# Kernel optimization log

Hardware: AMD Instinct MI355X
Metric: run time of the kernel (lower is better)

Reference implementation:

```python
import jax, jax.numpy as jnp
import numpy as np

KAPPA = 8
TEMP = 200.0
EPS = 1e-15
N, E, D, T = 8192, 131072, 128, 8
P0, P1 = 512, 128
ZI = D - KAPPA  # non-kappa feature dims


def expmap0(u):
    # Poincare ball exp map at origin, c=1
    n = jnp.clip(jnp.linalg.norm(u, axis=-1, keepdims=True), EPS)
    return jnp.tanh(n) * u / n


def logmap0(y):
    # Poincare ball log map at origin, c=1 (clipped for numerical safety)
    n = jnp.clip(jnp.linalg.norm(y, axis=-1, keepdims=True), EPS)
    t = jnp.clip(n, EPS, 1.0 - 1e-5)
    return jnp.arctanh(t) * y / n


def setup_inputs() -> dict:
    key = jax.random.key(0)
    ks = jax.random.split(key, 8)
    g = lambda k, shp: jax.random.normal(k, shp, jnp.float32) / np.float32(np.sqrt(shp[0]))
    return {
        "x": 0.1 * jax.random.normal(ks[0], (N, D), jnp.float32),
        "y": jax.random.normal(ks[1], (T, N), jnp.float32),
        "We0": g(ks[2], (ZI, ZI)), "be0": jnp.zeros((ZI,), jnp.float32),
        "Ws0": g(ks[3], (D, P0)), "bs0": jnp.zeros((P0,), jnp.float32),
        "We1": g(ks[4], (ZI, ZI)), "be1": jnp.zeros((ZI,), jnp.float32),
        "Ws1": g(ks[5], (D, P1)), "bs1": jnp.zeros((P1,), jnp.float32),
        "adj": jax.random.randint(ks[6], (2, E), 0, N),
    }


def _embed_pool(z, agg, We, be, Ws, bs):
    # embed_pool: keep z0, message-pass zi; compute cluster scores s (hyperbolic head)
    z0, zi = z[:, :KAPPA], z[:, KAPPA:]
    zi = agg(zi @ We + be)
    s = expmap0(agg(z @ Ws + bs))
    z = jnp.concatenate([z0, zi], axis=-1)
    S = jax.nn.softmax(logmap0(s) * TEMP, axis=0)  # soft assignment over nodes
    return z, S


def reference(x, y, We0, be0, Ws0, bs0, We1, be1, Ws1, bs1, adj):
    n = x.shape[0]
    # dense adjacency at level 0 (as in the original renorm)
    A0 = jnp.zeros((n, n), x.dtype).at[adj[0], adj[1]].set(1.0)
    # sparse aggregation equivalent to A0 @ h
    agg0 = lambda h: jax.ops.segment_sum(h[adj[1]], adj[0], num_segments=n)

    # ---- level 0 ----
    z, S0 = _embed_pool(x, agg0, We0, be0, Ws0, bs0)
    x1 = jnp.einsum('ij,ik->jk', S0, z)        # [P0, D] pooled features
    y1 = jnp.einsum('ij,ki->kj', S0, y)        # [T, P0] pooled targets
    A1 = jnp.einsum('ji,jk,kl->il', S0, A0, S0)  # [P0, P0] coarsened adjacency
    loss_ent = jax.scipy.special.entr(S0).sum()

    # ---- level 1 (dense weighted adjacency, i.e. dense_to_coo(A1) round trip) ----
    agg1 = lambda h: A1 @ h
    z1, S1 = _embed_pool(x1, agg1, We1, be1, Ws1, bs1)
    x2 = jnp.einsum('ij,ik->jk', S1, z1)       # [P1, D]
    y2 = jnp.einsum('ij,ki->kj', S1, y1)       # [T, P1]
    loss_ent = loss_ent + jax.scipy.special.entr(S1).sum()

    z_r = jnp.concatenate([x, x1, x2], axis=0)   # [N+P0+P1, D]
    y_r = jnp.concatenate([y, y1, y2], axis=-1)  # [T, N+P0+P1]
    return z_r, y_r, loss_ent
```

## Files before the change

### kernel.cpp

```cpp
#include <hip/hip_runtime.h>
#include <hip/hip_bf16.h>

#define NC   8192
#define EC   131072
#define DC   128
#define TC   8
#define P0C  512
#define P1C  128
#define ZIC  120
#define NCAT 248
#define TEMPC 200.0f
#define ATANH_MAX 6.1053405f

typedef short short8 __attribute__((ext_vector_type(8)));
typedef float f32x4 __attribute__((ext_vector_type(4)));

__device__ inline unsigned short f2b(float f) {
  union { float f; unsigned u; } x; x.f = f;
  unsigned r = x.u + 0x7FFFu + ((x.u >> 16) & 1u);
  return (unsigned short)(r >> 16);
}
__device__ inline float b2f(unsigned short b) {
  union { unsigned u; float f; } x; x.u = ((unsigned)b) << 16; return x.f;
}

__global__ void k_split_weights(const float* __restrict__ Ws0,
                                const float* __restrict__ We0,
                                unsigned short* __restrict__ WsHi,
                                unsigned short* __restrict__ WsLo,
                                unsigned short* __restrict__ WeHi,
                                unsigned short* __restrict__ WeLo)
{
  int idx = blockIdx.x * 256 + threadIdx.x;
  if (idx < P0C * DC) {
    int n = idx >> 7, k = idx & 127;
    float v = Ws0[(size_t)k * P0C + n];
    unsigned short h = f2b(v);
    WsHi[idx] = h; WsLo[idx] = f2b(v - b2f(h));
  } else if (idx < P0C * DC + DC * DC) {
    int j = idx - P0C * DC;
    int n = j >> 7, k = j & 127;
    float v = (n < ZIC && k >= 8) ? We0[(size_t)(k - 8) * ZIC + n] : 0.f;
    unsigned short h = f2b(v);
    WeHi[j] = h; WeLo[j] = f2b(v - b2f(h));
  }
}

__global__ void k_build_Bcat(const float* __restrict__ We1, const float* __restrict__ Ws1,
                             const float* __restrict__ be1, const float* __restrict__ bs1,
                             float* __restrict__ Bcat, float* __restrict__ bias_cat)
{
  int idx = blockIdx.x * 256 + threadIdx.x;
  const int total = DC * NCAT;
  if (idx < total) {
    int k = idx / NCAT, n = idx - k * NCAT;
    float v;
    if (n < ZIC) v = (k >= 8) ? We1[(size_t)(k - 8) * ZIC + n] : 0.f;
    else         v = Ws1[(size_t)k * P1C + (n - ZIC)];
    Bcat[idx] = v;
  } else if (idx < total + NCAT) {
    int n = idx - total;
    bias_cat[n] = (n < ZIC) ? be1[n] : bs1[n - ZIC];
  }
}

__global__ __launch_bounds__(256) void k_mfma_hilo(
    const unsigned short* __restrict__ Ahi, const unsigned short* __restrict__ Alo,
    const unsigned short* __restrict__ Bhi, const unsigned short* __restrict__ Blo,
    const float* __restrict__ bias, const float* __restrict__ degf,
    float* __restrict__ C, int ldc, int Nvalid)
{
  __shared__ unsigned short Ah[64][136], Al[64][136], Bh[64][136], Bl[64][136];
  const int bm = blockIdx.x * 64, bn = blockIdx.y * 64;
  const int tid = threadIdx.x;
  const int lane = tid & 63, wave = tid >> 6;
  const int lrow = lane & 15, lgrp = lane >> 4;
#pragma unroll
  for (int p = 0; p < 4; ++p) {
    int id = p * 256 + tid;
    int r = id >> 4, c = id & 15;
    *(uint4*)(&Ah[r][c * 8]) = *(const uint4*)(Ahi + (size_t)(bm + r) * 128 + c * 8);
    *(uint4*)(&Al[r][c * 8]) = *(const uint4*)(Alo + (size_t)(bm + r) * 128 + c * 8);
    *(uint4*)(&Bh[r][c * 8]) = *(const uint4*)(Bhi + (size_t)(bn + r) * 128 + c * 8);
    *(uint4*)(&Bl[r][c * 8]) = *(const uint4*)(Blo + (size_t)(bn + r) * 128 + c * 8);
  }
  __syncthreads();
  f32x4 acc[4];
#pragma unroll
  for (int nt = 0; nt < 4; ++nt) acc[nt] = (f32x4){0.f, 0.f, 0.f, 0.f};
#pragma unroll
  for (int kk = 0; kk < 4; ++kk) {
    short8 ah = *(const short8*)(&Ah[wave * 16 + lrow][kk * 32 + lgrp * 8]);
    short8 al = *(const short8*)(&Al[wave * 16 + lrow][kk * 32 + lgrp * 8]);
#pragma unroll
    for (int nt = 0; nt < 4; ++nt) {
      short8 bh = *(const short8*)(&Bh[nt * 16 + lrow][kk * 32 + lgrp * 8]);
      short8 bl = *(const short8*)(&Bl[nt * 16 + lrow][kk * 32 + lgrp * 8]);
      acc[nt] = __builtin_amdgcn_mfma_f32_16x16x32_bf16(ah, bh, acc[nt], 0, 0, 0);
      acc[nt] = __builtin_amdgcn_mfma_f32_16x16x32_bf16(ah, bl, acc[nt], 0, 0, 0);
      acc[nt] = __builtin_amdgcn_mfma_f32_16x16x32_bf16(al, bh, acc[nt], 0, 0, 0);
    }
  }
#pragma unroll
  for (int nt = 0; nt < 4; ++nt) {
    int n = bn + nt * 16 + lrow;
    if (n >= Nvalid) continue;
#pragma unroll
    for (int r = 0; r < 4; ++r) {
      int m = bm + wave * 16 + lgrp * 4 + r;
      C[(size_t)m * ldc + n] = acc[nt][r] + degf[m] * bias[n];
    }
  }
}

__global__ __launch_bounds__(256) void k_gemm_nn_part(
    const float* __restrict__ A, int lda,
    const float* __restrict__ B, int ldb,
    float* __restrict__ part,
    int M, int N, int K, int kchunk)
{
  __shared__ float As[16][65];
  __shared__ float Bs[16][65];
  int bm = blockIdx.x * 64, bn = blockIdx.y * 64;
  int z = blockIdx.z;
  int ks = z * kchunk, ke = min(K, ks + kchunk);
  int tid = threadIdx.x;
  int tm = (tid >> 4) << 2, tn = (tid & 15) << 2;
  float acc[4][4] = {};
  for (int k0 = ks; k0 < ke; k0 += 16) {
    for (int i = tid; i < 1024; i += 256) {
      int m = i >> 4, k = i & 15;
      float v = 0.f;
      if (bm + m < M && k0 + k < ke) v = A[(size_t)(bm + m) * lda + k0 + k];
      As[k][m] = v;
    }
    for (int i = tid; i < 1024; i += 256) {
      int k = i >> 6, n = i & 63;
      float v = 0.f;
      if (k0 + k < ke && bn + n < N) v = B[(size_t)(k0 + k) * ldb + bn + n];
      Bs[k][n] = v;
    }
    __syncthreads();
#pragma unroll
    for (int kk = 0; kk < 16; ++kk) {
      float a[4], b[4];
#pragma unroll
      for (int i = 0; i < 4; i++) a[i] = As[kk][tm + i];
#pragma unroll
      for (int j = 0; j < 4; j++) b[j] = Bs[kk][tn + j];
#pragma unroll
      for (int i = 0; i < 4; i++)
#pragma unroll
        for (int j = 0; j < 4; j++) acc[i][j] += a[i] * b[j];
    }
    __syncthreads();
  }
  size_t base = (size_t)z * M * N;
#pragma unroll
  for (int i = 0; i < 4; i++) {
    int m = bm + tm + i; if (m >= M) continue;
#pragma unroll
    for (int j = 0; j < 4; j++) {
      int n = bn + tn + j; if (n >= N) continue;
      part[base + (size_t)m * N + n] = acc[i][j];
    }
  }
}

__global__ void k_reduce_bias(const float* __restrict__ part,
                              const float* __restrict__ bias,
                              float* __restrict__ C, int nparts, int M, int N)
{
  int idx = blockIdx.x * 256 + threadIdx.x;
  if (idx >= M * N) return;
  int n = idx % N;
  float s = 0.f;
  for (int p = 0; p < nparts; ++p) s += part[(size_t)p * M * N + idx];
  if (bias) s += bias[n];
  C[idx] = s;
}

__global__ void k_reduce_stageB(const float* __restrict__ part,
                                const float* __restrict__ x1f,
                                float* __restrict__ z1, float* __restrict__ s1agg,
                                int nparts)
{
  int idx = blockIdx.x * 256 + threadIdx.x;
  const int MN = P0C * NCAT;
  if (idx < MN) {
    int m = idx / NCAT, n = idx - m * NCAT;
    float s = 0.f;
    for (int p = 0; p < nparts; ++p) s += part[(size_t)p * MN + idx];
    if (n < ZIC) z1[(size_t)m * DC + 8 + n] = s;
    else         s1agg[(size_t)m * P1C + (n - ZIC)] = s;
  } else if (idx < MN + P0C * 8) {
    int r = idx - MN; int m = r >> 3, c = r & 7;
    z1[(size_t)m * DC + c] = x1f[(size_t)m * DC + c];
  }
}

__global__ __launch_bounds__(256) void k_gemm_tn(
    const float* __restrict__ A, int lda,
    const float* __restrict__ B, int ldb,
    float* __restrict__ C, int ldc,
    int M, int N, int K, int kchunk)
{
  __shared__ float As[16][65];
  __shared__ float Bs[16][65];
  int bm = blockIdx.x * 64, bn = blockIdx.y * 64;
  int ks = blockIdx.z * kchunk;
  int ke = min(K, ks + kchunk);
  int tid = threadIdx.x;
  int tm = (tid >> 4) << 2, tn = (tid & 15) << 2;
  float acc[4][4] = {};
  for (int k0 = ks; k0 < ke; k0 += 16) {
    for (int i = tid; i < 1024; i += 256) {
      int k = i >> 6, m = i & 63;
      float v = 0.f;
      if (k0 + k < ke && bm + m < M) v = A[(size_t)(k0 + k) * lda + bm + m];
      As[k][m] = v;
    }
    for (int i = tid; i < 1024; i += 256) {
      int k = i >> 6, n = i & 63;
      float v = 0.f;
      if (k0 + k < ke && bn + n < N) v = B[(size_t)(k0 + k) * ldb + bn + n];
      Bs[k][n] = v;
    }
    __syncthreads();
#pragma unroll
    for (int kk = 0; kk < 16; ++kk) {
      float a[4], b[4];
#pragma unroll
      for (int i = 0; i < 4; i++) a[i] = As[kk][tm + i];
#pragma unroll
      for (int j = 0; j < 4; j++) b[j] = Bs[kk][tn + j];
#pragma unroll
      for (int i = 0; i < 4; i++)
#pragma unroll
        for (int j = 0; j < 4; j++) acc[i][j] += a[i] * b[j];
    }
    __syncthreads();
  }
#pragma unroll
  for (int i = 0; i < 4; i++) {
    int m = bm + tm + i; if (m >= M) continue;
#pragma unroll
    for (int j = 0; j < 4; j++) {
      int n = bn + tn + j; if (n >= N) continue;
      atomicAdd(&C[(size_t)m * ldc + n], acc[i][j]);
    }
  }
}

__global__ __launch_bounds__(256) void k_transpose_bf16(
    const float* __restrict__ src, int R, int C,
    unsigned short* __restrict__ dst)
{
  __shared__ float tile[64][65];
  int br = blockIdx.x * 64, bc = blockIdx.y * 64;
  for (int idx = threadIdx.x; idx < 4096; idx += 256) {
    int r = idx >> 6, c = idx & 63;
    tile[r][c] = src[(size_t)(br + r) * C + bc + c];
  }
  __syncthreads();
  for (int idx = threadIdx.x; idx < 4096; idx += 256) {
    int c = idx >> 6, r = idx & 63;
    dst[(size_t)(bc + c) * R + br + r] = f2b(tile[r][c]);
  }
}

__global__ __launch_bounds__(256) void k_transpose_b2b(
    const unsigned short* __restrict__ src, int R, int C,
    unsigned short* __restrict__ dst)
{
  __shared__ unsigned short tile[64][65];
  int br = blockIdx.x * 64, bc = blockIdx.y * 64;
  for (int idx = threadIdx.x; idx < 4096; idx += 256) {
    int r = idx >> 6, c = idx & 63;
    tile[r][c] = src[(size_t)(br + r) * C + bc + c];
  }
  __syncthreads();
  for (int idx = threadIdx.x; idx < 4096; idx += 256) {
    int c = idx >> 6, r = idx & 63;
    dst[(size_t)(bc + c) * R + br + r] = tile[r][c];
  }
}

__global__ __launch_bounds__(256) void k_nt_bf16(
    const unsigned short* __restrict__ At,
    const unsigned short* __restrict__ Bt,
    float* __restrict__ Cpart,
    int M, int N, int K, int kchunk)
{
  __shared__ unsigned short Alds[64][136];
  __shared__ unsigned short Blds[64][136];
  const int bm = blockIdx.x * 64, bn = blockIdx.y * 64;
  const int z = blockIdx.z;
  const int k_beg = z * kchunk, k_end = k_beg + kchunk;
  const int tid = threadIdx.x;
  const int lane = tid & 63, wave = tid >> 6;
  const int lrow = lane & 15, lgrp = lane >> 4;
  f32x4 acc[4];
#pragma unroll
  for (int nt = 0; nt < 4; ++nt) acc[nt] = (f32x4){0.f, 0.f, 0.f, 0.f};

  for (int k0 = k_beg; k0 < k_end; k0 += 128) {
#pragma unroll
    for (int p = 0; p < 4; ++p) {
      int id = p * 256 + tid;
      int r = id >> 4;
      int c = id & 15;
      *(uint4*)(&Alds[r][c * 8]) =
          *(const uint4*)(At + (size_t)(bm + r) * K + k0 + c * 8);
      *(uint4*)(&Blds[r][c * 8]) =
          *(const uint4*)(Bt + (size_t)(bn + r) * K + k0 + c * 8);
    }
    __syncthreads();
#pragma unroll
    for (int kk = 0; kk < 4; ++kk) {
      short8 af = *(const short8*)(&Alds[wave * 16 + lrow][kk * 32 + lgrp * 8]);
#pragma unroll
      for (int nt = 0; nt < 4; ++nt) {
        short8 bf = *(const short8*)(&Blds[nt * 16 + lrow][kk * 32 + lgrp * 8]);
        acc[nt] = __builtin_amdgcn_mfma_f32_16x16x32_bf16(af, bf, acc[nt], 0, 0, 0);
      }
    }
    __syncthreads();
  }
  size_t base = (size_t)z * M * N;
#pragma unroll
  for (int nt = 0; nt < 4; ++nt) {
    int n = bn + nt * 16 + lrow;
#pragma unroll
    for (int r = 0; r < 4; ++r) {
      int m = bm + wave * 16 + lgrp * 4 + r;
      Cpart[base + (size_t)m * N + n] = acc[nt][r];
    }
  }
}

__global__ void k_reduce_parts(const float* __restrict__ part, float* __restrict__ C,
                               int nparts, int sz)
{
  int idx = blockIdx.x * 256 + threadIdx.x;
  if (idx >= sz) return;
  float s = 0.f;
  for (int p = 0; p < nparts; ++p) s += part[(size_t)p * sz + idx];
  C[idx] = s;
}

__global__ void k_count(const int* __restrict__ adj, int* __restrict__ counts)
{
  int e = blockIdx.x * 256 + threadIdx.x;
  if (e < EC) atomicAdd(&counts[adj[e]], 1);
}

__global__ __launch_bounds__(1024) void k_scan(const int* __restrict__ counts,
                                               int* __restrict__ offsets,
                                               float* __restrict__ degf)
{
  __shared__ int tsum[1024];
  int tid = threadIdx.x;
  int base = tid * 8;
  int loc[8]; int s = 0;
#pragma unroll
  for (int i = 0; i < 8; i++) { loc[i] = s; s += counts[base + i]; }
  tsum[tid] = s;
  __syncthreads();
  for (int off = 1; off < 1024; off <<= 1) {
    int v = (tid >= off) ? tsum[tid - off] : 0;
    __syncthreads();
    tsum[tid] += v;
    __syncthreads();
  }
  int excl = (tid == 0) ? 0 : tsum[tid - 1];
#pragma unroll
  for (int i = 0; i < 8; i++) {
    offsets[base + i] = excl + loc[i];
    degf[base + i] = (float)counts[base + i];
  }
  if (tid == 1023) offsets[NC] = tsum[1023];
}

__global__ void k_scatter(const int* __restrict__ adj, const int* __restrict__ offsets,
                          int* __restrict__ fill, int* __restrict__ csr)
{
  int e = blockIdx.x * 256 + threadIdx.x;
  if (e < EC) {
    int d = adj[e], s = adj[EC + e];
    int p = atomicAdd(&fill[d], 1);
    csr[offsets[d] + p] = s;
  }
}

__global__ __launch_bounds__(128) void k_aggX(
    const int* __restrict__ offsets, const int* __restrict__ csr,
    const float* __restrict__ x,
    float* __restrict__ xa, float* __restrict__ z,
    unsigned short* __restrict__ hi, unsigned short* __restrict__ lo)
{
  int j = blockIdx.x;
  int beg = offsets[j], deg = offsets[j + 1] - beg;
  __shared__ int srcs[512];
  bool inl = (deg <= 512);
  if (inl) for (int i = threadIdx.x; i < deg; i += 128) srcs[i] = csr[beg + i];
  __syncthreads();
  int c = threadIdx.x;
  float acc = 0.f;
  if (inl) {
    int i = 0;
    for (; i + 4 <= deg; i += 4) {
      int s0 = srcs[i], s1 = srcs[i+1], s2 = srcs[i+2], s3 = srcs[i+3];
      float v0 = x[(size_t)s0 * DC + c], v1 = x[(size_t)s1 * DC + c];
      float v2 = x[(size_t)s2 * DC + c], v3 = x[(size_t)s3 * DC + c];
      acc += v0; acc += v1; acc += v2; acc += v3;
    }
    for (; i < deg; ++i) acc += x[(size_t)srcs[i] * DC + c];
  } else {
    for (int i = 0; i < deg; ++i) acc += x[(size_t)csr[beg + i] * DC + c];
  }
  xa[(size_t)j * DC + c] = acc;
  unsigned short h = f2b(acc);
  hi[(size_t)j * DC + c] = h;
  lo[(size_t)j * DC + c] = f2b(acc - b2f(h));
  if (c < 8) z[(size_t)j * DC + c] = x[(size_t)j * DC + c];
}

__global__ __launch_bounds__(256) void k_aggM_bf16(
    const int* __restrict__ offsets, const int* __restrict__ csr,
    const unsigned short* __restrict__ S0h, unsigned short* __restrict__ Mbh)
{
  int j = blockIdx.x;
  int beg = offsets[j], deg = offsets[j + 1] - beg;
  __shared__ int srcs[512];
  __shared__ int nv_s;
  bool inl = (deg <= 512);
  if (inl) for (int i = threadIdx.x; i < deg; i += 256) srcs[i] = csr[beg + i];
  __syncthreads();
  if (inl) {
    for (int t = threadIdx.x; t < deg; t += 256) {
      int v = srcs[t];
      for (int u = 0; u < t; ++u)
        if (csr[beg + u] == v) { srcs[t] = -1; break; }
    }
  }
  __syncthreads();
  if (threadIdx.x == 0) {
    int nv = 0;
    if (inl) {
      for (int i = 0; i < deg; i++) if (srcs[i] >= 0) srcs[nv++] = srcs[i];
    }
    nv_s = nv;
  }
  __syncthreads();
  int c2 = threadIdx.x;
  float a0 = 0.f, a1 = 0.f;
  if (inl) {
    int nv = nv_s;
    int i = 0;
    for (; i + 4 <= nv; i += 4) {
      int s0 = srcs[i], s1 = srcs[i+1], s2 = srcs[i+2], s3 = srcs[i+3];
      ushort2 v0 = *(const ushort2*)(S0h + (size_t)s0 * P0C + c2 * 2);
      ushort2 v1 = *(const ushort2*)(S0h + (size_t)s1 * P0C + c2 * 2);
      ushort2 v2 = *(const ushort2*)(S0h + (size_t)s2 * P0C + c2 * 2);
      ushort2 v3 = *(const ushort2*)(S0h + (size_t)s3 * P0C + c2 * 2);
      a0 += b2f(v0.x); a1 += b2f(v0.y);
      a0 += b2f(v1.x); a1 += b2f(v1.y);
      a0 += b2f(v2.x); a1 += b2f(v2.y);
      a0 += b2f(v3.x); a1 += b2f(v3.y);
    }
    for (; i < nv; ++i) {
      ushort2 v = *(const ushort2*)(S0h + (size_t)srcs[i] * P0C + c2 * 2);
      a0 += b2f(v.x); a1 += b2f(v.y);
    }
  } else {
    for (int i = 0; i < deg; i++) {
      int s = csr[beg + i];
      bool dup = false;
      for (int u = 0; u < i; u++) if (csr[beg + u] == s) { dup = true; break; }
      if (!dup) {
        ushort2 v = *(const ushort2*)(S0h + (size_t)s * P0C + c2 * 2);
        a0 += b2f(v.x); a1 += b2f(v.y);
      }
    }
  }
  ushort2 o2; o2.x = f2b(a0); o2.y = f2b(a1);
  *(ushort2*)(Mbh + (size_t)j * P0C + c2 * 2) = o2;
}

__global__ __launch_bounds__(256) void k_rowscale(const float* __restrict__ U, int cols,
                                                  float* __restrict__ rs)
{
  int r = blockIdx.x;
  const float* row = U + (size_t)r * cols;
  float ss = 0.f;
  for (int c = threadIdx.x; c < cols; c += 256) { float v = row[c]; ss += v * v; }
  for (int off = 32; off > 0; off >>= 1) ss += __shfl_down(ss, off);
  __shared__ float red[4];
  if ((threadIdx.x & 63) == 0) red[threadIdx.x >> 6] = ss;
  __syncthreads();
  if (threadIdx.x == 0) {
    float n = sqrtf(red[0] + red[1] + red[2] + red[3]);
    n = fmaxf(n, 1e-15f);
    rs[r] = TEMPC * fminf(n, ATANH_MAX) / n;
  }
}

__global__ __launch_bounds__(256) void k_smaxA(const float* __restrict__ U,
    const float* __restrict__ rs, float* __restrict__ pm, float* __restrict__ ps,
    int rows, int cols, int rpg)
{
  int lc = threadIdx.x & 63;
  int c = blockIdx.x * 64 + lc;
  int rl = threadIdx.x >> 6;
  int r0 = blockIdx.y * rpg, r1 = min(rows, r0 + rpg);
  float m = -1e30f, s = 0.f;
  for (int r = r0 + rl; r < r1; r += 4) {
    float l = rs[r] * U[(size_t)r * cols + c];
    if (l > m) { s = s * __expf(m - l) + 1.f; m = l; }
    else s += __expf(l - m);
  }
  __shared__ float sm[4][64], sv[4][64];
  sm[rl][lc] = m; sv[rl][lc] = s;
  __syncthreads();
  if (threadIdx.x < 64) {
    float mm = sm[0][threadIdx.x], s2 = sv[0][threadIdx.x];
    for (int q = 1; q < 4; q++) {
      float mq = sm[q][threadIdx.x], sq = sv[q][threadIdx.x];
      float mn = fmaxf(mm, mq);
      s2 = s2 * __expf(mm - mn) + sq * __expf(mq - mn);
      mm = mn;
    }
    pm[(size_t)blockIdx.y * cols + blockIdx.x * 64 + threadIdx.x] = mm;
    ps[(size_t)blockIdx.y * cols + blockIdx.x * 64 + threadIdx.x] = s2;
  }
}

__global__ void k_smaxB(const float* __restrict__ pm, const float* __restrict__ ps,
                        float* __restrict__ colm, float* __restrict__ colsum,
                        int ng, int cols)
{
  int c = blockIdx.x * blockDim.x + threadIdx.x;
  if (c >= cols) return;
  float m = -1e30f, s = 0.f;
  for (int g = 0; g < ng; g++) {
    float mg = pm[(size_t)g * cols + c], sg = ps[(size_t)g * cols + c];
    float mn = fmaxf(m, mg);
    s = s * __expf(m - mn) + sg * __expf(mg - mn);
    m = mn;
  }
  colm[c] = m; colsum[c] = s;
}

__global__ __launch_bounds__(256) void k_smaxC(const float* __restrict__ U,
    const float* __restrict__ rs, const float* __restrict__ colm,
    const float* __restrict__ colsum, float* __restrict__ S,
    unsigned short* __restrict__ Sh,
    float* __restrict__ loss, int rows, int cols, int rpg)
{
  int lc = threadIdx.x & 63;
  int c = blockIdx.x * 64 + lc;
  int rl = threadIdx.x >> 6;
  int r0 = blockIdx.y * rpg, r1 = min(rows, r0 + rpg);
  float m = colm[c], inv = 1.f / colsum[c];
  float h = 0.f;
  for (int r = r0 + rl; r < r1; r += 4) {
    float l = rs[r] * U[(size_t)r * cols + c];
    float p = __expf(l - m) * inv;
    S[(size_t)r * cols + c] = p;
    Sh[(size_t)r * cols + c] = f2b(p);
    if (p > 0.f) h -= p * __logf(p);
  }
  for (int off = 32; off > 0; off >>= 1) h += __shfl_down(h, off);
  __shared__ float red[4];
  if ((threadIdx.x & 63) == 0) red[threadIdx.x >> 6] = h;
  __syncthreads();
  if (threadIdx.x == 0) atomicAdd(loss, red[0] + red[1] + red[2] + red[3]);
}

__global__ __launch_bounds__(256) void k_smax_col(const float* __restrict__ U,
    const float* __restrict__ rs, float* __restrict__ S, float* __restrict__ loss,
    int rows, int cols)
{
  int c = blockIdx.x;
  int tid = threadIdx.x;
  int r0 = tid, r1 = tid + 256;
  float v0 = rs[r0] * U[(size_t)r0 * cols + c];
  float v1 = rs[r1] * U[(size_t)r1 * cols + c];
  float m = fmaxf(v0, v1);
  for (int off = 32; off > 0; off >>= 1) m = fmaxf(m, __shfl_xor(m, off));
  __shared__ float red[4];
  if ((tid & 63) == 0) red[tid >> 6] = m;
  __syncthreads();
  m = fmaxf(fmaxf(red[0], red[1]), fmaxf(red[2], red[3]));
  float e0 = __expf(v0 - m), e1 = __expf(v1 - m);
  float s = e0 + e1;
  for (int off = 32; off > 0; off >>= 1) s += __shfl_xor(s, off);
  __syncthreads();
  __shared__ float red2[4];
  if ((tid & 63) == 0) red2[tid >> 6] = s;
  __syncthreads();
  s = red2[0] + red2[1] + red2[2] + red2[3];
  float inv = 1.f / s;
  float p0 = e0 * inv, p1 = e1 * inv;
  S[(size_t)r0 * cols + c] = p0;
  S[(size_t)r1 * cols + c] = p1;
  float h = 0.f;
  if (p0 > 0.f) h -= p0 * __logf(p0);
  if (p1 > 0.f) h -= p1 * __logf(p1);
  for (int off = 32; off > 0; off >>= 1) h += __shfl_xor(h, off);
  __syncthreads();
  __shared__ float red3[4];
  if ((tid & 63) == 0) red3[tid >> 6] = h;
  __syncthreads();
  if (tid == 0) atomicAdd(loss, red3[0] + red3[1] + red3[2] + red3[3]);
}

__global__ __launch_bounds__(256) void k_yS_part(
    const float* __restrict__ Y, int ldy,
    const float* __restrict__ S, int ldS,
    float* __restrict__ part, int K, int C, int kchunk)
{
  int lc = threadIdx.x & 63;
  int c = blockIdx.x * 64 + lc;
  int rl = threadIdx.x >> 6;
  int r0 = blockIdx.y * kchunk, r1 = min(K, r0 + kchunk);
  float acc[8] = {};
  for (int r = r0 + rl; r < r1; r += 4) {
    float sv = S[(size_t)r * ldS + c];
#pragma unroll
    for (int t = 0; t < 8; t++) acc[t] += Y[(size_t)t * ldy + r] * sv;
  }
  __shared__ float red[4][8][64];
#pragma unroll
  for (int t = 0; t < 8; t++) red[rl][t][lc] = acc[t];
  __syncthreads();
  if (rl == 0) {
#pragma unroll
    for (int t = 0; t < 8; t++) {
      float v = red[0][t][lc] + red[1][t][lc] + red[2][t][lc] + red[3][t][lc];
      part[((size_t)blockIdx.y * 8 + t) * C + c] = v;
    }
  }
}

__global__ void k_yS_red(const float* __restrict__ part, float* __restrict__ outp,
                         int nparts, int sz)
{
  int idx = blockIdx.x * 256 + threadIdx.x;
  if (idx >= sz) return;
  float s = 0.f;
  for (int p = 0; p < nparts; ++p) s += part[(size_t)p * sz + idx];
  outp[idx] = s;
}

__global__ void k_emit_all(const float* __restrict__ x, const float* __restrict__ x1f,
                           const float* __restrict__ x2f, const float* __restrict__ y,
                           const float* __restrict__ y1f, const float* __restrict__ y2f,
                           const float* __restrict__ lossf, float* __restrict__ out,
                           int total)
{
  int idx = blockIdx.x * 256 + threadIdx.x;
  if (idx >= total) return;
  float v;
  if (idx < 1048576) v = x[idx];
  else if (idx < 1114112) v = x1f[idx - 1048576];
  else if (idx < 1130496) v = x2f[idx - 1114112];
  else if (idx < 1201152) {
    int r = idx - 1130496;
    int t = r / 8832, c = r - t * 8832;
    if (c < 8192) v = y[(size_t)t * 8192 + c];
    else if (c < 8704) v = y1f[t * 512 + (c - 8192)];
    else v = y2f[t * 128 + (c - 8704)];
  } else v = lossf[0];
  out[idx] = v;
}

extern "C" void kernel_launch(void* const* d_in, const int* in_sizes, int n_in,
                              void* d_out, int out_size, void* d_ws, size_t ws_size,
                              hipStream_t stream)
{
  (void)in_sizes; (void)n_in; (void)ws_size;
  const float* x   = (const float*)d_in[0];
  const float* y   = (const float*)d_in[1];
  const float* We0 = (const float*)d_in[2];
  const float* be0 = (const float*)d_in[3];
  const float* Ws0 = (const float*)d_in[4];
  const float* bs0 = (const float*)d_in[5];
  const float* We1 = (const float*)d_in[6];
  const float* be1 = (const float*)d_in[7];
  const float* Ws1 = (const float*)d_in[8];
  const float* bs1 = (const float*)d_in[9];
  const int*   adj = (const int*)d_in[10];
  float* out = (float*)d_out;

  float* ws = (float*)d_ws;
  size_t o = 0;
  auto alloc = [&](size_t n) { float* p = ws + o; o += n; return p; };
  float* xa    = alloc((size_t)NC * DC);
  float* sPre  = alloc((size_t)NC * P0C);
  float* sAgg  = alloc((size_t)NC * P0C);
  float* zbuf  = alloc((size_t)NC * DC);
  float* rsc   = alloc(NC);
  float* degf  = alloc(NC);
  float* pm    = alloc(32 * P0C);
  float* ps    = alloc(32 * P0C);
  float* colm  = alloc(P0C);
  float* colsum= alloc(P0C);
  float* s1agg = alloc((size_t)P0C * P1C);
  float* S1    = alloc((size_t)P0C * P1C);
  float* z1    = alloc((size_t)P0C * P1C);
  float* rs1   = alloc(P0C);
  float* x1f   = alloc((size_t)P0C * DC);
  float* A1    = alloc((size_t)P0C * P0C);
  unsigned short* S0T   = (unsigned short*)alloc((size_t)P0C * NC / 2);
  unsigned short* MbT   = (unsigned short*)alloc((size_t)P0C * NC / 2);
  unsigned short* zbufT = (unsigned short*)alloc((size_t)DC * NC / 2);
  unsigned short* S0h   = (unsigned short*)alloc((size_t)NC * P0C / 2);
  unsigned short* xaHi  = (unsigned short*)alloc((size_t)NC * DC / 2);
  unsigned short* xaLo  = (unsigned short*)alloc((size_t)NC * DC / 2);
  unsigned short* WsHi  = (unsigned short*)alloc((size_t)P0C * DC / 2);
  unsigned short* WsLo  = (unsigned short*)alloc((size_t)P0C * DC / 2);
  unsigned short* WeHi  = (unsigned short*)alloc((size_t)DC * DC / 2);
  unsigned short* WeLo  = (unsigned short*)alloc((size_t)DC * DC / 2);
  float* Bcat   = alloc((size_t)DC * NCAT);
  float* biascat= alloc(NCAT);
  float* t1s1   = alloc((size_t)P0C * NCAT);
  float* partSA = alloc((size_t)4 * P0C * NCAT);
  float* partSB = alloc((size_t)8 * P0C * NCAT);
  float* partY1 = alloc((size_t)128 * TC * P0C);
  float* partY2 = alloc((size_t)8 * TC * P1C);
  float* x2f   = alloc((size_t)P1C * DC);
  float* y1f   = alloc((size_t)TC * P0C);
  float* y2f   = alloc((size_t)TC * P1C);
  float* lossf = alloc(1);
  size_t atomicFloats = (size_t)P1C*DC + (size_t)TC*P0C + (size_t)TC*P1C + 1;
  o = (o + 63) & ~(size_t)63;
  int* ibase   = (int*)(ws + o);
  int* counts  = ibase;
  int* fill    = ibase + NC;
  int* offsets = ibase + 2 * NC;
  int* csr     = ibase + 2 * NC + (NC + 1);

  float* S0 = sPre;
  unsigned short* Mbh = (unsigned short*)sAgg;
  float* partsA1 = sAgg + (size_t)2 * 1024 * 1024;
  float* partsX1 = zbuf;

  hipMemsetAsync(x2f, 0, atomicFloats * sizeof(float), stream);
  hipMemsetAsync(counts, 0, 2 * NC * sizeof(int), stream);

  k_count  <<<EC/256, 256, 0, stream>>>(adj, counts);
  k_scan   <<<1, 1024, 0, stream>>>(counts, offsets, degf);
  k_scatter<<<EC/256, 256, 0, stream>>>(adj, offsets, fill, csr);
  k_split_weights<<<(P0C*DC + DC*DC + 255)/256, 256, 0, stream>>>(Ws0, We0, WsHi, WsLo, WeHi, WeLo);
  k_build_Bcat<<<(DC*NCAT + NCAT + 255)/256, 256, 0, stream>>>(We1, Ws1, be1, bs1, Bcat, biascat);

  k_aggX<<<NC, 128, 0, stream>>>(offsets, csr, x, xa, zbuf, xaHi, xaLo);
  k_mfma_hilo<<<dim3(NC/64, P0C/64), 256, 0, stream>>>(xaHi, xaLo, WsHi, WsLo, bs0, degf, sAgg, P0C, P0C);
  k_mfma_hilo<<<dim3(NC/64, 2), 256, 0, stream>>>(xaHi, xaLo, WeHi, WeLo, be0, degf, zbuf + 8, DC, ZIC);
  k_transpose_bf16<<<dim3(NC/64, DC/64), 256, 0, stream>>>(zbuf, NC, DC, zbufT);

  k_rowscale<<<NC, 256, 0, stream>>>(sAgg, P0C, rsc);
  k_smaxA<<<dim3(P0C/64, 32), 256, 0, stream>>>(sAgg, rsc, pm, ps, NC, P0C, 256);
  k_smaxB<<<P0C/256, 256, 0, stream>>>(pm, ps, colm, colsum, 32, P0C);
  k_smaxC<<<dim3(P0C/64, 32), 256, 0, stream>>>(sAgg, rsc, colm, colsum, S0, S0h, lossf, NC, P0C, 256);
  k_transpose_bf16<<<dim3(NC/64, P0C/64), 256, 0, stream>>>(S0, NC, P0C, S0T);

  k_aggM_bf16<<<NC, 256, 0, stream>>>(offsets, csr, S0h, Mbh);
  k_transpose_b2b<<<dim3(NC/64, P0C/64), 256, 0, stream>>>(Mbh, NC, P0C, MbT);

  k_nt_bf16<<<dim3(P0C/64, P0C/64, 8), 256, 0, stream>>>(S0T, MbT, partsA1, P0C, P0C, NC, 1024);
  k_reduce_parts<<<(P0C*P0C)/256, 256, 0, stream>>>(partsA1, A1, 8, P0C*P0C);
  k_nt_bf16<<<dim3(P0C/64, DC/64, 16), 256, 0, stream>>>(S0T, zbufT, partsX1, P0C, DC, NC, 512);
  k_reduce_parts<<<(P0C*DC)/256, 256, 0, stream>>>(partsX1, x1f, 16, P0C*DC);
  k_yS_part<<<dim3(P0C/64, 128), 256, 0, stream>>>(y, NC, S0, P0C, partY1, NC, P0C, 64);
  k_yS_red<<<(TC*P0C + 255)/256, 256, 0, stream>>>(partY1, y1f, 128, TC*P0C);

  k_gemm_nn_part<<<dim3(P0C/64, 4, 4), 256, 0, stream>>>(x1f, DC, Bcat, NCAT, partSA, P0C, NCAT, DC, 32);
  k_reduce_bias<<<(P0C*NCAT + 255)/256, 256, 0, stream>>>(partSA, biascat, t1s1, 4, P0C, NCAT);
  k_gemm_nn_part<<<dim3(P0C/64, 4, 8), 256, 0, stream>>>(A1, P0C, t1s1, NCAT, partSB, P0C, NCAT, P0C, 64);
  k_reduce_stageB<<<(P0C*NCAT + P0C*8 + 255)/256, 256, 0, stream>>>(partSB, x1f, z1, s1agg, 8);

  k_rowscale<<<P0C, 256, 0, stream>>>(s1agg, P1C, rs1);
  k_smax_col<<<P1C, 256, 0, stream>>>(s1agg, rs1, S1, lossf, P0C, P1C);
  k_gemm_tn<<<dim3(P1C/64, DC/64, 16), 256, 0, stream>>>(S1, P1C, z1, DC, x2f, DC, P1C, DC, P0C, 32);
  k_yS_part<<<dim3(P1C/64, 8), 256, 0, stream>>>(y1f, P0C, S1, P1C, partY2, P0C, P1C, 64);
  k_yS_red<<<(TC*P1C + 255)/256, 256, 0, stream>>>(partY2, y2f, 8, TC*P1C);

  k_emit_all<<<(out_size + 255)/256, 256, 0, stream>>>(x, x1f, x2f, y, y1f, y2f, lossf, out, out_size);
}
```

Measured before the change: 308.3 us.

## Fuse weight prep, merge level-0 GEMMs, and fuse S0 transpose into softmax

Combines the two weight-prep kernels into one and concatenates Ws0 and We0 so a single hi/lo MFMA GEMM writes both the score and embedding outputs. The softmax finalize kernel now writes only bf16 S0 and produces the transposed S0T through a shared-memory tile, which removes the fp32 S0 buffer and the separate transpose kernel. The y·S0 reduction reads the bf16 S0, and the neighbour aggregation loop is unrolled to 8. These changes cut launches and fp32 memory traffic, at the cost of bf16 rounding in the y pooling and a larger shared-memory footprint in the softmax kernel.

Measured after the change: 304.8 us. About the same (-1.1%).

```diff
diff --git a/kernel.cpp b/kernel.cpp
--- a/kernel.cpp
+++ b/kernel.cpp
@@ -9,6 +9,7 @@
 #define P1C  128
 #define ZIC  120
 #define NCAT 248
+#define NW0  640
 #define TEMPC 200.0f
 #define ATANH_MAX 6.1053405f
 
@@ -24,51 +25,50 @@
   union { unsigned u; float f; } x; x.u = ((unsigned)b) << 16; return x.f;
 }
 
-__global__ void k_split_weights(const float* __restrict__ Ws0,
-                                const float* __restrict__ We0,
-                                unsigned short* __restrict__ WsHi,
-                                unsigned short* __restrict__ WsLo,
-                                unsigned short* __restrict__ WeHi,
-                                unsigned short* __restrict__ WeLo)
+__global__ void k_prep(const float* __restrict__ Ws0, const float* __restrict__ We0,
+                       const float* __restrict__ bs0, const float* __restrict__ be0,
+                       const float* __restrict__ We1, const float* __restrict__ Ws1,
+                       const float* __restrict__ be1, const float* __restrict__ bs1,
+                       unsigned short* __restrict__ WcatHi, unsigned short* __restrict__ WcatLo,
+                       float* __restrict__ bias0cat,
+                       float* __restrict__ Bcat, float* __restrict__ biascat1)
 {
   int idx = blockIdx.x * 256 + threadIdx.x;
-  if (idx < P0C * DC) {
+  const int A = NW0 * DC;
+  const int B = A + NW0;
+  const int Cc = B + DC * NCAT;
+  const int Dd = Cc + NCAT;
+  if (idx < A) {
     int n = idx >> 7, k = idx & 127;
-    float v = Ws0[(size_t)k * P0C + n];
+    float v;
+    if (n < P0C) v = Ws0[(size_t)k * P0C + n];
+    else {
+      int nn = n - P0C;
+      v = (nn < ZIC && k >= 8) ? We0[(size_t)(k - 8) * ZIC + nn] : 0.f;
+    }
     unsigned short h = f2b(v);
-    WsHi[idx] = h; WsLo[idx] = f2b(v - b2f(h));
-  } else if (idx < P0C * DC + DC * DC) {
-    int j = idx - P0C * DC;
-    int n = j >> 7, k = j & 127;
-    float v = (n < ZIC && k >= 8) ? We0[(size_t)(k - 8) * ZIC + n] : 0.f;
-    unsigned short h = f2b(v);
-    WeHi[j] = h; WeLo[j] = f2b(v - b2f(h));
-  }
-}
-
-__global__ void k_build_Bcat(const float* __restrict__ We1, const float* __restrict__ Ws1,
-                             const float* __restrict__ be1, const float* __restrict__ bs1,
-                             float* __restrict__ Bcat, float* __restrict__ bias_cat)
-{
-  int idx = blockIdx.x * 256 + threadIdx.x;
-  const int total = DC * NCAT;
-  if (idx < total) {
-    int k = idx / NCAT, n = idx - k * NCAT;
+    WcatHi[idx] = h; WcatLo[idx] = f2b(v - b2f(h));
+  } else if (idx < B) {
+    int n = idx - A;
+    bias0cat[n] = (n < P0C) ? bs0[n] : ((n - P0C) < ZIC ? be0[n - P0C] : 0.f);
+  } else if (idx < Cc) {
+    int j = idx - B;
+    int k = j / NCAT, n = j - k * NCAT;
     float v;
     if (n < ZIC) v = (k >= 8) ? We1[(size_t)(k - 8) * ZIC + n] : 0.f;
     else         v = Ws1[(size_t)k * P1C + (n - ZIC)];
-    Bcat[idx] = v;
-  } else if (idx < total + NCAT) {
-    int n = idx - total;
-    bias_cat[n] = (n < ZIC) ? be1[n] : bs1[n - ZIC];
-  }
-}
-
-__global__ __launch_bounds__(256) void k_mfma_hilo(
+    Bcat[j] = v;
+  } else if (idx < Dd) {
+    int n = idx - Cc;
+    biascat1[n] = (n < ZIC) ? be1[n] : bs1[n - ZIC];
+  }
+}
+
+__global__ __launch_bounds__(256) void k_mfma_hilo2(
     const unsigned short* __restrict__ Ahi, const unsigned short* __restrict__ Alo,
     const unsigned short* __restrict__ Bhi, const unsigned short* __restrict__ Blo,
     const float* __restrict__ bias, const float* __restrict__ degf,
-    float* __restrict__ C, int ldc, int Nvalid)
+    float* __restrict__ C0, float* __restrict__ C1)
 {
   __shared__ unsigned short Ah[64][136], Al[64][136], Bh[64][136], Bl[64][136];
   const int bm = blockIdx.x * 64, bn = blockIdx.y * 64;
@@ -104,11 +104,12 @@
 #pragma unroll
   for (int nt = 0; nt < 4; ++nt) {
     int n = bn + nt * 16 + lrow;
-    if (n >= Nvalid) continue;
 #pragma unroll
     for (int r = 0; r < 4; ++r) {
       int m = bm + wave * 16 + lgrp * 4 + r;
-      C[(size_t)m * ldc + n] = acc[nt][r] + degf[m] * bias[n];
+      float v = acc[nt][r] + degf[m] * bias[n];
+      if (n < P0C) C0[(size_t)m * P0C + n] = v;
+      else if (n - P0C < ZIC) C1[(size_t)m * DC + 8 + (n - P0C)] = v;
     }
   }
 }
@@ -458,16 +459,19 @@
   if (inl) {
     int nv = nv_s;
     int i = 0;
-    for (; i + 4 <= nv; i += 4) {
-      int s0 = srcs[i], s1 = srcs[i+1], s2 = srcs[i+2], s3 = srcs[i+3];
-      ushort2 v0 = *(const ushort2*)(S0h + (size_t)s0 * P0C + c2 * 2);
-      ushort2 v1 = *(const ushort2*)(S0h + (size_t)s1 * P0C + c2 * 2);
-      ushort2 v2 = *(const ushort2*)(S0h + (size_t)s2 * P0C + c2 * 2);
-      ushort2 v3 = *(const ushort2*)(S0h + (size_t)s3 * P0C + c2 * 2);
-      a0 += b2f(v0.x); a1 += b2f(v0.y);
-      a0 += b2f(v1.x); a1 += b2f(v1.y);
-      a0 += b2f(v2.x); a1 += b2f(v2.y);
-      a0 += b2f(v3.x); a1 += b2f(v3.y);
+    for (; i + 8 <= nv; i += 8) {
+      ushort2 v0 = *(const ushort2*)(S0h + (size_t)srcs[i]   * P0C + c2 * 2);
+      ushort2 v1 = *(const ushort2*)(S0h + (size_t)srcs[i+1] * P0C + c2 * 2);
+      ushort2 v2 = *(const ushort2*)(S0h + (size_t)srcs[i+2] * P0C + c2 * 2);
+      ushort2 v3 = *(const ushort2*)(S0h + (size_t)srcs[i+3] * P0C + c2 * 2);
+      ushort2 v4 = *(const ushort2*)(S0h + (size_t)srcs[i+4] * P0C + c2 * 2);
+      ushort2 v5 = *(const ushort2*)(S0h + (size_t)srcs[i+5] * P0C + c2 * 2);
+      ushort2 v6 = *(const ushort2*)(S0h + (size_t)srcs[i+6] * P0C + c2 * 2);
+      ushort2 v7 = *(const ushort2*)(S0h + (size_t)srcs[i+7] * P0C + c2 * 2);
+      a0 += b2f(v0.x) + b2f(v1.x) + b2f(v2.x) + b2f(v3.x)
+          + b2f(v4.x) + b2f(v5.x) + b2f(v6.x) + b2f(v7.x);
+      a1 += b2f(v0.y) + b2f(v1.y) + b2f(v2.y) + b2f(v3.y)
+          + b2f(v4.y) + b2f(v5.y) + b2f(v6.y) + b2f(v7.y);
     }
     for (; i < nv; ++i) {
       ushort2 v = *(const ushort2*)(S0h + (size_t)srcs[i] * P0C + c2 * 2);
@@ -554,28 +558,36 @@
 
 __global__ __launch_bounds__(256) void k_smaxC(const float* __restrict__ U,
     const float* __restrict__ rs, const float* __restrict__ colm,
-    const float* __restrict__ colsum, float* __restrict__ S,
-    unsigned short* __restrict__ Sh,
-    float* __restrict__ loss, int rows, int cols, int rpg)
-{
+    const float* __restrict__ colsum,
+    unsigned short* __restrict__ Sh, unsigned short* __restrict__ ST,
+    float* __restrict__ loss, int rows, int cols)
+{
+  __shared__ unsigned short tile[64][258];
+  __shared__ float red[4];
   int lc = threadIdx.x & 63;
-  int c = blockIdx.x * 64 + lc;
+  int gc = blockIdx.x * 64 + lc;
   int rl = threadIdx.x >> 6;
-  int r0 = blockIdx.y * rpg, r1 = min(rows, r0 + rpg);
-  float m = colm[c], inv = 1.f / colsum[c];
+  int r0 = blockIdx.y * 256;
+  float m = colm[gc], inv = 1.f / colsum[gc];
   float h = 0.f;
-  for (int r = r0 + rl; r < r1; r += 4) {
-    float l = rs[r] * U[(size_t)r * cols + c];
+  for (int rr = rl; rr < 256; rr += 4) {
+    int r = r0 + rr;
+    float l = rs[r] * U[(size_t)r * cols + gc];
     float p = __expf(l - m) * inv;
-    S[(size_t)r * cols + c] = p;
-    Sh[(size_t)r * cols + c] = f2b(p);
+    unsigned short pb = f2b(p);
+    Sh[(size_t)r * cols + gc] = pb;
+    tile[lc][rr] = pb;
     if (p > 0.f) h -= p * __logf(p);
   }
   for (int off = 32; off > 0; off >>= 1) h += __shfl_down(h, off);
-  __shared__ float red[4];
   if ((threadIdx.x & 63) == 0) red[threadIdx.x >> 6] = h;
   __syncthreads();
   if (threadIdx.x == 0) atomicAdd(loss, red[0] + red[1] + red[2] + red[3]);
+  int gc0 = blockIdx.x * 64;
+  for (int idx = threadIdx.x; idx < 64 * 256; idx += 256) {
+    int col = idx >> 8, rr = idx & 255;
+    ST[(size_t)(gc0 + col) * rows + r0 + rr] = tile[col][rr];
+  }
 }
 
 __global__ __launch_bounds__(256) void k_smax_col(const float* __restrict__ U,
@@ -628,6 +640,34 @@
   float acc[8] = {};
   for (int r = r0 + rl; r < r1; r += 4) {
     float sv = S[(size_t)r * ldS + c];
+#pragma unroll
+    for (int t = 0; t < 8; t++) acc[t] += Y[(size_t)t * ldy + r] * sv;
+  }
+  __shared__ float red[4][8][64];
+#pragma unroll
+  for (int t = 0; t < 8; t++) red[rl][t][lc] = acc[t];
+  __syncthreads();
+  if (rl == 0) {
+#pragma unroll
+    for (int t = 0; t < 8; t++) {
+      float v = red[0][t][lc] + red[1][t][lc] + red[2][t][lc] + red[3][t][lc];
+      part[((size_t)blockIdx.y * 8 + t) * C + c] = v;
+    }
+  }
+}
+
+__global__ __launch_bounds__(256) void k_yS_part_b(
+    const float* __restrict__ Y, int ldy,
+    const unsigned short* __restrict__ S, int ldS,
+    float* __restrict__ part, int K, int C, int kchunk)
+{
+  int lc = threadIdx.x & 63;
+  int c = blockIdx.x * 64 + lc;
+  int rl = threadIdx.x >> 6;
+  int r0 = blockIdx.y * kchunk, r1 = min(K, r0 + kchunk);
+  float acc[8] = {};
+  for (int r = r0 + rl; r < r1; r += 4) {
+    float sv = b2f(S[(size_t)r * ldS + c]);
 #pragma unroll
     for (int t = 0; t < 8; t++) acc[t] += Y[(size_t)t * ldy + r] * sv;
   }
@@ -698,7 +738,6 @@
   size_t o = 0;
   auto alloc = [&](size_t n) { float* p = ws + o; o += n; return p; };
   float* xa    = alloc((size_t)NC * DC);
-  float* sPre  = alloc((size_t)NC * P0C);
   float* sAgg  = alloc((size_t)NC * P0C);
   float* zbuf  = alloc((size_t)NC * DC);
   float* rsc   = alloc(NC);
@@ -719,12 +758,11 @@
   unsigned short* S0h   = (unsigned short*)alloc((size_t)NC * P0C / 2);
   unsigned short* xaHi  = (unsigned short*)alloc((size_t)NC * DC / 2);
   unsigned short* xaLo  = (unsigned short*)alloc((size_t)NC * DC / 2);
-  unsigned short* WsHi  = (unsigned short*)alloc((size_t)P0C * DC / 2);
-  unsigned short* WsLo  = (unsigned short*)alloc((size_t)P0C * DC / 2);
-  unsigned short* WeHi  = (unsigned short*)alloc((size_t)DC * DC / 2);
-  unsigned short* WeLo  = (unsigned short*)alloc((size_t)DC * DC / 2);
+  unsigned short* WcatHi= (unsigned short*)alloc((size_t)NW0 * DC / 2);
+  unsigned short* WcatLo= (unsigned short*)alloc((size_t)NW0 * DC / 2);
+  float* bias0cat = alloc(NW0);
   float* Bcat   = alloc((size_t)DC * NCAT);
-  float* biascat= alloc(NCAT);
+  float* biascat1= alloc(NCAT);
   float* t1s1   = alloc((size_t)P0C * NCAT);
   float* partSA = alloc((size_t)4 * P0C * NCAT);
   float* partSB = alloc((size_t)8 * P0C * NCAT);
@@ -742,7 +780,6 @@
   int* offsets = ibase + 2 * NC;
   int* csr     = ibase + 2 * NC + (NC + 1);
 
-  float* S0 = sPre;
   unsigned short* Mbh = (unsigned short*)sAgg;
   float* partsA1 = sAgg + (size_t)2 * 1024 * 1024;
   float* partsX1 = zbuf;
@@ -753,19 +790,19 @@
   k_count  <<<EC/256, 256, 0, stream>>>(adj, counts);
   k_scan   <<<1, 1024, 0, stream>>>(counts, offsets, degf);
   k_scatter<<<EC/256, 256, 0, stream>>>(adj, offsets, fill, csr);
-  k_split_weights<<<(P0C*DC + DC*DC + 255)/256, 256, 0, stream>>>(Ws0, We0, WsHi, WsLo, WeHi, WeLo);
-  k_build_Bcat<<<(DC*NCAT + NCAT + 255)/256, 256, 0, stream>>>(We1, Ws1, be1, bs1, Bcat, biascat);
+  k_prep<<<(NW0*DC + NW0 + DC*NCAT + NCAT + 255)/256, 256, 0, stream>>>(
+      Ws0, We0, bs0, be0, We1, Ws1, be1, bs1,
+      WcatHi, WcatLo, bias0cat, Bcat, biascat1);
 
   k_aggX<<<NC, 128, 0, stream>>>(offsets, csr, x, xa, zbuf, xaHi, xaLo);
-  k_mfma_hilo<<<dim3(NC/64, P0C/64), 256, 0, stream>>>(xaHi, xaLo, WsHi, WsLo, bs0, degf, sAgg, P0C, P0C);
-  k_mfma_hilo<<<dim3(NC/64, 2), 256, 0, stream>>>(xaHi, xaLo, WeHi, WeLo, be0, degf, zbuf + 8, DC, ZIC);
+  k_mfma_hilo2<<<dim3(NC/64, NW0/64), 256, 0, stream>>>(xaHi, xaLo, WcatHi, WcatLo,
+                                                        bias0cat, degf, sAgg, zbuf);
   k_transpose_bf16<<<dim3(NC/64, DC/64), 256, 0, stream>>>(zbuf, NC, DC, zbufT);
 
   k_rowscale<<<NC, 256, 0, stream>>>(sAgg, P0C, rsc);
   k_smaxA<<<dim3(P0C/64, 32), 256, 0, stream>>>(sAgg, rsc, pm, ps, NC, P0C, 256);
   k_smaxB<<<P0C/256, 256, 0, stream>>>(pm, ps, colm, colsum, 32, P0C);
-  k_smaxC<<<dim3(P0C/64, 32), 256, 0, stream>>>(sAgg, rsc, colm, colsum, S0, S0h, lossf, NC, P0C, 256);
-  k_transpose_bf16<<<dim3(NC/64, P0C/64), 256, 0, stream>>>(S0, NC, P0C, S0T);
+  k_smaxC<<<dim3(P0C/64, 32), 256, 0, stream>>>(sAgg, rsc, colm, colsum, S0h, S0T, lossf, NC, P0C);
 
   k_aggM_bf16<<<NC, 256, 0, stream>>>(offsets, csr, S0h, Mbh);
   k_transpose_b2b<<<dim3(NC/64, P0C/64), 256, 0, stream>>>(Mbh, NC, P0C, MbT);
@@ -774,11 +811,11 @@
   k_reduce_parts<<<(P0C*P0C)/256, 256, 0, stream>>>(partsA1, A1, 8, P0C*P0C);
   k_nt_bf16<<<dim3(P0C/64, DC/64, 16), 256, 0, stream>>>(S0T, zbufT, partsX1, P0C, DC, NC, 512);
   k_reduce_parts<<<(P0C*DC)/256, 256, 0, stream>>>(partsX1, x1f, 16, P0C*DC);
-  k_yS_part<<<dim3(P0C/64, 128), 256, 0, stream>>>(y, NC, S0, P0C, partY1, NC, P0C, 64);
+  k_yS_part_b<<<dim3(P0C/64, 128), 256, 0, stream>>>(y, NC, S0h, P0C, partY1, NC, P0C, 64);
   k_yS_red<<<(TC*P0C + 255)/256, 256, 0, stream>>>(partY1, y1f, 128, TC*P0C);
 
   k_gemm_nn_part<<<dim3(P0C/64, 4, 4), 256, 0, stream>>>(x1f, DC, Bcat, NCAT, partSA, P0C, NCAT, DC, 32);
-  k_reduce_bias<<<(P0C*NCAT + 255)/256, 256, 0, stream>>>(partSA, biascat, t1s1, 4, P0C, NCAT);
+  k_reduce_bias<<<(P0C*NCAT + 255)/256, 256, 0, stream>>>(partSA, biascat1, t1s1, 4, P0C, NCAT);
   k_gemm_nn_part<<<dim3(P0C/64, 4, 8), 256, 0, stream>>>(A1, P0C, t1s1, NCAT, partSB, P0C, NCAT, P0C, 64);
   k_reduce_stageB<<<(P0C*NCAT + P0C*8 + 255)/256, 256, 0, stream>>>(partSB, x1f, z1, s1agg, 8);
 
```
